# Kernel optimization log

Hardware: AMD Instinct MI355X
Metric: run time of the kernel (lower is better)

Reference implementation:

```python
import jax, jax.numpy as jnp
import numpy as np

SEQ_LEN = 4096
INPUT_SIZE = 1024
OUTPUT_SIZE = 1024


def _xavier(key, shape):
    n = shape[0]
    lim = 1.0 / (n ** 0.5)
    return jax.random.uniform(key, shape, minval=-lim, maxval=lim, dtype=jnp.float32)


def setup_inputs() -> dict:
    key = jax.random.key(0)
    kx, kk, kv, kq = jax.random.split(key, 4)
    X = jax.random.normal(kx, (SEQ_LEN, INPUT_SIZE), dtype=jnp.float32)
    Wk = _xavier(kk, (INPUT_SIZE, OUTPUT_SIZE))
    Wv = _xavier(kv, (INPUT_SIZE, OUTPUT_SIZE))
    Wq = _xavier(kq, (INPUT_SIZE, OUTPUT_SIZE))
    return {"X": X, "Wk": Wk, "Wv": Wv, "Wq": Wq}


def reference(X, Wk, Wv, Wq):
    # Faithful to original: scores = K @ Q^T (note K first, no 1/sqrt(d) scaling)
    K = X @ Wk  # (S, D)
    V = X @ Wv  # (S, D)
    Q = X @ Wq  # (S, D)
    scores = jnp.einsum('sd,td->st', K, Q)  # (S, S) == K @ Q^T
    attn = jax.nn.softmax(scores, axis=-1) @ V  # (S, D)
    return attn
```

## Files before the change

### kernel.cpp

```cpp
#include <hip/hip_runtime.h>
#include <hip/hip_fp16.h>
#include <cstdint>

#define SEQ 4096
#define DIM 1024

typedef _Float16 f16x8 __attribute__((ext_vector_type(8)));
typedef float f32x16 __attribute__((ext_vector_type(16)));
typedef __attribute__((address_space(1))) void as1_void;
typedef __attribute__((address_space(3))) void as3_void;

__device__ __forceinline__ ushort f2h(float f) {
  _Float16 h = (_Float16)f;
  return __builtin_bit_cast(ushort, h);
}

__global__ void convert_all_kernel(const float* __restrict__ X, const float* __restrict__ Wk,
                                   const float* __restrict__ Wv, const float* __restrict__ Wq,
                                   ushort* __restrict__ Xh, ushort* __restrict__ Wt) {
  const int z = blockIdx.z;
  const int tx = threadIdx.x, ty = threadIdx.y;
  if (z == 3) {
    const int bid = blockIdx.y * 32 + blockIdx.x;
    const int t = ty * 32 + tx;
#pragma unroll
    for (int k = 0; k < 4; k++) {
      int i = bid * 1024 + k * 256 + t;
      float4 v = reinterpret_cast<const float4*>(X)[i];
      ushort4 o = { f2h(v.x), f2h(v.y), f2h(v.z), f2h(v.w) };
      reinterpret_cast<ushort4*>(Xh)[i] = o;
    }
    return;
  }
  __shared__ float tile[32][33];
  const float* W = (z == 0) ? Wk : (z == 1) ? Wv : Wq;
  int n0 = blockIdx.x * 32, k0 = blockIdx.y * 32;
#pragma unroll
  for (int r = 0; r < 4; r++) {
    int k = ty + r * 8;
    tile[k][tx] = W[(size_t)(k0 + k) * DIM + n0 + tx];
  }
  __syncthreads();
  ushort* out = Wt + (size_t)z * DIM * DIM;
#pragma unroll
  for (int r = 0; r < 4; r++) {
    int n = ty + r * 8;
    out[(size_t)(n0 + n) * DIM + k0 + tx] = f2h(tile[tx][n]);
  }
}

template <bool F16_OUT>
__device__ __forceinline__ void gemm_tile(const ushort* __restrict__ A,
                                          const ushort* __restrict__ B,
                                          void* __restrict__ C,
                                          int N, int K, int m0, int n0,
                                          int kt0, int ktend) {
  constexpr int BK = 64;
  __shared__ __align__(16) ushort As[128 * BK];
  __shared__ __align__(16) ushort Bs[128 * BK];
  const int tid = threadIdx.x;
  const int wave = tid >> 6, lane = tid & 63;
  const int l31 = lane & 31, khalf = lane >> 5;
  const int wm = (wave & 1) * 64, wn = (wave >> 1) * 64;

  const int srow = tid >> 3;
  const int skey = ((srow & 7) ^ ((srow >> 3) & 3));
  const int sce = (((tid & 7) ^ skey) * 8);
  const int rk = (l31 & 7) ^ ((l31 >> 3) & 3);

  f32x16 acc[2][2];
#pragma unroll
  for (int i = 0; i < 2; i++)
#pragma unroll
    for (int j = 0; j < 2; j++)
#pragma unroll
      for (int r = 0; r < 16; r++) acc[i][j][r] = 0.f;

  for (int kt = kt0; kt < ktend; kt += BK) {
    __syncthreads();
#pragma unroll
    for (int q = 0; q < 4; q++) {
      const ushort* ga = A + (size_t)(m0 + srow + q * 32) * K + kt + sce;
      __builtin_amdgcn_global_load_lds((const as1_void*)ga,
                                       (as3_void*)&As[wave * 512 + q * 2048], 16, 0, 0);
    }
#pragma unroll
    for (int q = 0; q < 4; q++) {
      const ushort* gb = B + (size_t)(n0 + srow + q * 32) * K + kt + sce;
      __builtin_amdgcn_global_load_lds((const as1_void*)gb,
                                       (as3_void*)&Bs[wave * 512 + q * 2048], 16, 0, 0);
    }
    __syncthreads();
#pragma unroll
    for (int ks = 0; ks < 4; ks++) {
      f16x8 af[2], bfr[2];
      const int ck = (ks * 2 + khalf);
#pragma unroll
      for (int i = 0; i < 2; i++)
        af[i] = *reinterpret_cast<const f16x8*>(
            &As[(wm + i * 32 + l31) * BK + ((ck ^ rk) * 8)]);
#pragma unroll
      for (int j = 0; j < 2; j++)
        bfr[j] = *reinterpret_cast<const f16x8*>(
            &Bs[(wn + j * 32 + l31) * BK + ((ck ^ rk) * 8)]);
#pragma unroll
      for (int i = 0; i < 2; i++)
#pragma unroll
        for (int j = 0; j < 2; j++)
          acc[i][j] = __builtin_amdgcn_mfma_f32_32x32x16_f16(af[i], bfr[j], acc[i][j], 0, 0, 0);
    }
  }

#pragma unroll
  for (int i = 0; i < 2; i++)
#pragma unroll
    for (int j = 0; j < 2; j++)
#pragma unroll
      for (int r = 0; r < 16; r++) {
        int row = m0 + wm + i * 32 + (r & 3) + 8 * (r >> 2) + 4 * khalf;
        int col = n0 + wn + j * 32 + l31;
        if (F16_OUT)
          reinterpret_cast<ushort*>(C)[(size_t)row * N + col] = f2h(acc[i][j][r]);
        else
          reinterpret_cast<float*>(C)[(size_t)row * N + col] = acc[i][j][r];
      }
}

__device__ __forceinline__ void gemm_tile_w128(const ushort* __restrict__ A,
                                               const ushort* __restrict__ B,
                                               ushort* __restrict__ C,
                                               int N, int K, int m0, int n0,
                                               int kt0, int ktend) {
  constexpr int BK = 64;
  __shared__ __align__(16) ushort As[128 * BK];
  __shared__ __align__(16) ushort Bs[256 * BK];
  const int tid = threadIdx.x;
  const int wave = tid >> 6, lane = tid & 63;
  const int l31 = lane & 31, khalf = lane >> 5;
  const int wm = (wave & 1) * 64, wn = (wave >> 1) * 128;

  const int srow = tid >> 3;
  const int skey = ((srow & 7) ^ ((srow >> 3) & 3));
  const int sce = (((tid & 7) ^ skey) * 8);
  const int rk = (l31 & 7) ^ ((l31 >> 3) & 3);

  f32x16 acc[2][4];
#pragma unroll
  for (int i = 0; i < 2; i++)
#pragma unroll
    for (int j = 0; j < 4; j++)
#pragma unroll
      for (int r = 0; r < 16; r++) acc[i][j][r] = 0.f;

  for (int kt = kt0; kt < ktend; kt += BK) {
    __syncthreads();
#pragma unroll
    for (int q = 0; q < 4; q++) {
      const ushort* ga = A + (size_t)(m0 + srow + q * 32) * K + kt + sce;
      __builtin_amdgcn_global_load_lds((const as1_void*)ga,
                                       (as3_void*)&As[wave * 512 + q * 2048], 16, 0, 0);
    }
#pragma unroll
    for (int q = 0; q < 8; q++) {
      const ushort* gb = B + (size_t)(n0 + srow + q * 32) * K + kt + sce;
      __builtin_amdgcn_global_load_lds((const as1_void*)gb,
                                       (as3_void*)&Bs[wave * 512 + q * 2048], 16, 0, 0);
    }
    __syncthreads();
#pragma unroll
    for (int ks = 0; ks < 4; ks++) {
      f16x8 af[2], bfr[4];
      const int ck = (ks * 2 + khalf);
#pragma unroll
      for (int i = 0; i < 2; i++)
        af[i] = *reinterpret_cast<const f16x8*>(
            &As[(wm + i * 32 + l31) * BK + ((ck ^ rk) * 8)]);
#pragma unroll
      for (int j = 0; j < 4; j++)
        bfr[j] = *reinterpret_cast<const f16x8*>(
            &Bs[(wn + j * 32 + l31) * BK + ((ck ^ rk) * 8)]);
#pragma unroll
      for (int i = 0; i < 2; i++)
#pragma unroll
        for (int j = 0; j < 4; j++)
          acc[i][j] = __builtin_amdgcn_mfma_f32_32x32x16_f16(af[i], bfr[j], acc[i][j], 0, 0, 0);
    }
  }

#pragma unroll
  for (int i = 0; i < 2; i++)
#pragma unroll
    for (int j = 0; j < 4; j++)
#pragma unroll
      for (int r = 0; r < 16; r++) {
        int row = m0 + wm + i * 32 + (r & 3) + 8 * (r >> 2) + 4 * khalf;
        int col = n0 + wn + j * 32 + l31;
        C[(size_t)row * N + col] = f2h(acc[i][j][r]);
      }
}

__global__ __launch_bounds__(256) void proj_kernel(const ushort* __restrict__ Xh,
                                                   const ushort* __restrict__ Wt,
                                                   ushort* __restrict__ Kh,
                                                   ushort* __restrict__ Qh,
                                                   ushort* __restrict__ Vt) {
  const int z = blockIdx.z;
  const ushort* A;
  const ushort* B;
  ushort* C;
  int N, m0, n0;
  if (z < 2) {
    A = Xh;
    B = Wt + (size_t)(z == 0 ? 0 : 2) * DIM * DIM;
    C = (z == 0) ? Kh : Qh;
    N = DIM;
    m0 = (blockIdx.x >> 3) * 128;
    n0 = (blockIdx.x & 7) * 128;
  } else {
    A = Wt + (size_t)DIM * DIM;
    B = Xh;
    C = Vt;
    N = SEQ;
    m0 = (blockIdx.x >> 5) * 128;
    n0 = (blockIdx.x & 31) * 128;
  }
  gemm_tile<true>(A, B, C, N, DIM, m0, n0, 0, DIM);
}

__global__ __launch_bounds__(256, 2) void score_kernel(const ushort* __restrict__ Kh,
                                                       const ushort* __restrict__ Qh,
                                                       ushort* __restrict__ S) {
  const int f = blockIdx.x;
  const int xcd = f & 7;
  const int r = f >> 3;
  const int t = xcd * 64 + r;
  const int within = t & 63, st = t >> 6;
  const int sx = within & 7, sy = within >> 3;
  const int tx = (st & 1) * 8 + sx;
  const int ty = (st >> 1) * 8 + sy;
  gemm_tile_w128(Kh, Qh, S, SEQ, DIM, ty * 128, tx * 256, 0, DIM);
}

__global__ __launch_bounds__(256, 2) void out_splitk_kernel(const ushort* __restrict__ P,
                                                            const ushort* __restrict__ Vt,
                                                            ushort* __restrict__ Part) {
  const int f = blockIdx.x;
  const int z = f >> 7;
  const int q = f & 127;
  const int xcd = q & 7;
  const int r = q >> 3;
  const int t = xcd * 16 + r;
  const int tx = t & 3, ty = t >> 2;
  ushort* C = Part + (size_t)z * SEQ * DIM;
  gemm_tile_w128(P, Vt, C, DIM, SEQ, ty * 128, tx * 256,
                 z * (SEQ / 4), (z + 1) * (SEQ / 4));
}

__global__ void reduce4_kernel(const ushort* __restrict__ Part, float* __restrict__ out, int n8) {
  int i = blockIdx.x * blockDim.x + threadIdx.x;
  if (i >= n8) return;
  const f16x8* p0 = reinterpret_cast<const f16x8*>(Part);
  const f16x8* p1 = p0 + n8;
  const f16x8* p2 = p1 + n8;
  const f16x8* p3 = p2 + n8;
  f16x8 a = p0[i], b = p1[i], c = p2[i], d = p3[i];
  float4 lo, hi;
  lo.x = (float)a[0] + (float)b[0] + (float)c[0] + (float)d[0];
  lo.y = (float)a[1] + (float)b[1] + (float)c[1] + (float)d[1];
  lo.z = (float)a[2] + (float)b[2] + (float)c[2] + (float)d[2];
  lo.w = (float)a[3] + (float)b[3] + (float)c[3] + (float)d[3];
  hi.x = (float)a[4] + (float)b[4] + (float)c[4] + (float)d[4];
  hi.y = (float)a[5] + (float)b[5] + (float)c[5] + (float)d[5];
  hi.z = (float)a[6] + (float)b[6] + (float)c[6] + (float)d[6];
  hi.w = (float)a[7] + (float)b[7] + (float)c[7] + (float)d[7];
  reinterpret_cast<float4*>(out)[i * 2] = lo;
  reinterpret_cast<float4*>(out)[i * 2 + 1] = hi;
}

__global__ __launch_bounds__(256) void softmax_kernel(const ushort* __restrict__ S,
                                                      ushort* __restrict__ P) {
  const int wave = threadIdx.x >> 6, lane = threadIdx.x & 63;
  const int row = blockIdx.x * 4 + wave;
  const ushort* s = S + (size_t)row * SEQ;
  float v[64];
#pragma unroll
  for (int i = 0; i < 8; i++) {
    f16x8 h = reinterpret_cast<const f16x8*>(s)[i * 64 + lane];
#pragma unroll
    for (int j = 0; j < 8; j++) v[i * 8 + j] = (float)h[j];
  }
  float m = v[0];
#pragma unroll
  for (int j = 1; j < 64; j++) m = fmaxf(m, v[j]);
#pragma unroll
  for (int o = 32; o > 0; o >>= 1) m = fmaxf(m, __shfl_xor(m, o, 64));
  float sum = 0.f;
#pragma unroll
  for (int j = 0; j < 64; j++) {
    v[j] = __expf(v[j] - m);
    sum += v[j];
  }
#pragma unroll
  for (int o = 32; o > 0; o >>= 1) sum += __shfl_xor(sum, o, 64);
  float inv = 1.0f / sum;
  ushort* p = P + (size_t)row * SEQ;
#pragma unroll
  for (int i = 0; i < 8; i++) {
    f16x8 h;
#pragma unroll
    for (int j = 0; j < 8; j++) h[j] = (_Float16)(v[i * 8 + j] * inv);
    reinterpret_cast<f16x8*>(p)[i * 64 + lane] = h;
  }
}

extern "C" void kernel_launch(void* const* d_in, const int* in_sizes, int n_in,
                              void* d_out, int out_size, void* d_ws, size_t ws_size,
                              hipStream_t stream) {
  const float* X = (const float*)d_in[0];
  const float* Wk = (const float*)d_in[1];
  const float* Wv = (const float*)d_in[2];
  const float* Wq = (const float*)d_in[3];

  char* ws = (char*)d_ws;
  size_t off = 0;
  ushort* Xh = (ushort*)(ws + off); off += (size_t)SEQ * DIM * 2;
  ushort* Wt = (ushort*)(ws + off); off += (size_t)3 * DIM * DIM * 2;
  ushort* Kh = (ushort*)(ws + off); off += (size_t)SEQ * DIM * 2;
  ushort* Qh = (ushort*)(ws + off); off += (size_t)SEQ * DIM * 2;
  ushort* Vt = (ushort*)(ws + off); off += (size_t)SEQ * DIM * 2;
  ushort* S = (ushort*)(ws + off);  off += (size_t)SEQ * SEQ * 2;
  ushort* P = (ushort*)(ws + off);  off += (size_t)SEQ * SEQ * 2;

  ushort* Part = S;

  convert_all_kernel<<<dim3(32, 32, 4), dim3(32, 8), 0, stream>>>(X, Wk, Wv, Wq, Xh, Wt);
  proj_kernel<<<dim3(256, 1, 3), 256, 0, stream>>>(Xh, Wt, Kh, Qh, Vt);
  score_kernel<<<512, 256, 0, stream>>>(Kh, Qh, S);
  softmax_kernel<<<1024, 256, 0, stream>>>(S, P);
  out_splitk_kernel<<<512, 256, 0, stream>>>(P, Vt, Part);
  reduce4_kernel<<<SEQ * DIM / 8 / 256, 256, 0, stream>>>(Part, (float*)d_out, SEQ * DIM / 8);
}
```

Baseline: 210.2 us.

## Use 256x256 double-buffered GEMM tiles with 8 waves for all GEMMs

Replaces the two 128-row GEMM tile routines with a single 256x256 tile routine that runs 512 threads (8 waves, each computing 128x64) and double-buffers the A and B tiles in LDS. The loads for the next K slice are issued during the MFMA phase, with per-step barriers and setprio raised around the MFMAs. The projection, score and output GEMMs all switch to this tile and to new launch grids with XCD-aware block remapping. The aim is more data reuse per tile and load/compute overlap; the cost is 128KB of LDS per block, which limits occupancy, and fewer blocks (256) per launch, which can underfill the CUs.

```diff
diff --git a/kernel.cpp b/kernel.cpp
--- a/kernel.cpp
+++ b/kernel.cpp
@@ -49,148 +49,94 @@
   }
 }
 
-template <bool F16_OUT>
-__device__ __forceinline__ void gemm_tile(const ushort* __restrict__ A,
-                                          const ushort* __restrict__ B,
-                                          void* __restrict__ C,
-                                          int N, int K, int m0, int n0,
-                                          int kt0, int ktend) {
+__device__ __forceinline__ void gemm_tile256(const ushort* __restrict__ A,
+                                             const ushort* __restrict__ B,
+                                             ushort* __restrict__ C,
+                                             int N, int K, int m0, int n0,
+                                             int kt0, int ktend) {
   constexpr int BK = 64;
-  __shared__ __align__(16) ushort As[128 * BK];
-  __shared__ __align__(16) ushort Bs[128 * BK];
+  __shared__ __align__(16) ushort As[2][256 * BK];
+  __shared__ __align__(16) ushort Bs[2][256 * BK];
   const int tid = threadIdx.x;
   const int wave = tid >> 6, lane = tid & 63;
   const int l31 = lane & 31, khalf = lane >> 5;
-  const int wm = (wave & 1) * 64, wn = (wave >> 1) * 64;
+  const int wm = (wave & 1) * 128, wn = (wave >> 1) * 64;
 
   const int srow = tid >> 3;
   const int skey = ((srow & 7) ^ ((srow >> 3) & 3));
   const int sce = (((tid & 7) ^ skey) * 8);
   const int rk = (l31 & 7) ^ ((l31 >> 3) & 3);
 
-  f32x16 acc[2][2];
-#pragma unroll
-  for (int i = 0; i < 2; i++)
+  f32x16 acc[4][2];
+#pragma unroll
+  for (int i = 0; i < 4; i++)
 #pragma unroll
     for (int j = 0; j < 2; j++)
 #pragma unroll
       for (int r = 0; r < 16; r++) acc[i][j][r] = 0.f;
 
-  for (int kt = kt0; kt < ktend; kt += BK) {
-    __syncthreads();
-#pragma unroll
-    for (int q = 0; q < 4; q++) {
-      const ushort* ga = A + (size_t)(m0 + srow + q * 32) * K + kt + sce;
-      __builtin_amdgcn_global_load_lds((const as1_void*)ga,
-                                       (as3_void*)&As[wave * 512 + q * 2048], 16, 0, 0);
-    }
-#pragma unroll
-    for (int q = 0; q < 4; q++) {
-      const ushort* gb = B + (size_t)(n0 + srow + q * 32) * K + kt + sce;
-      __builtin_amdgcn_global_load_lds((const as1_void*)gb,
-                                       (as3_void*)&Bs[wave * 512 + q * 2048], 16, 0, 0);
+  const ushort* Abase = A + (size_t)(m0 + srow) * K + sce;
+  const ushort* Bbase = B + (size_t)(n0 + srow) * K + sce;
+  const int ldsbase = wave * 512;
+
+#pragma unroll
+  for (int q = 0; q < 4; q++)
+    __builtin_amdgcn_global_load_lds((const as1_void*)(Abase + (size_t)q * 64 * K + kt0),
+                                     (as3_void*)&As[0][ldsbase + q * 4096], 16, 0, 0);
+#pragma unroll
+  for (int q = 0; q < 4; q++)
+    __builtin_amdgcn_global_load_lds((const as1_void*)(Bbase + (size_t)q * 64 * K + kt0),
+                                     (as3_void*)&Bs[0][ldsbase + q * 4096], 16, 0, 0);
+  __syncthreads();
+
+  const int ntiles = (ktend - kt0) >> 6;
+  for (int tt = 0; tt < ntiles; ++tt) {
+    const int cur = tt & 1;
+    const int kt = kt0 + tt * BK;
+    const bool pf = (tt + 1 < ntiles);
+    const ushort* As_c = As[cur];
+    const ushort* Bs_c = Bs[cur];
+#pragma unroll
+    for (int ks = 0; ks < 4; ks++) {
+      f16x8 af[4], bf2[2];
+      const int co = (((ks * 2 + khalf) ^ rk) * 8);
+#pragma unroll
+      for (int i = 0; i < 4; i++)
+        af[i] = *reinterpret_cast<const f16x8*>(&As_c[(wm + i * 32 + l31) * BK + co]);
+#pragma unroll
+      for (int j = 0; j < 2; j++)
+        bf2[j] = *reinterpret_cast<const f16x8*>(&Bs_c[(wn + j * 32 + l31) * BK + co]);
+      if (pf && ks == 0) {
+#pragma unroll
+        for (int q = 0; q < 4; q++)
+          __builtin_amdgcn_global_load_lds(
+              (const as1_void*)(Abase + (size_t)q * 64 * K + kt + BK),
+              (as3_void*)&As[cur ^ 1][ldsbase + q * 4096], 16, 0, 0);
+      }
+      if (pf && ks == 1) {
+#pragma unroll
+        for (int q = 0; q < 4; q++)
+          __builtin_amdgcn_global_load_lds(
+              (const as1_void*)(Bbase + (size_t)q * 64 * K + kt + BK),
+              (as3_void*)&Bs[cur ^ 1][ldsbase + q * 4096], 16, 0, 0);
+      }
+      __builtin_amdgcn_s_barrier();
+      __builtin_amdgcn_s_setprio(1);
+#pragma unroll
+      for (int i = 0; i < 4; i++)
+#pragma unroll
+        for (int j = 0; j < 2; j++)
+          acc[i][j] = __builtin_amdgcn_mfma_f32_32x32x16_f16(af[i], bf2[j], acc[i][j], 0, 0, 0);
+      __builtin_amdgcn_s_setprio(0);
+      if (ks < 3) __builtin_amdgcn_s_barrier();
     }
     __syncthreads();
-#pragma unroll
-    for (int ks = 0; ks < 4; ks++) {
-      f16x8 af[2], bfr[2];
-      const int ck = (ks * 2 + khalf);
-#pragma unroll
-      for (int i = 0; i < 2; i++)
-        af[i] = *reinterpret_cast<const f16x8*>(
-            &As[(wm + i * 32 + l31) * BK + ((ck ^ rk) * 8)]);
-#pragma unroll
-      for (int j = 0; j < 2; j++)
-        bfr[j] = *reinterpret_cast<const f16x8*>(
-            &Bs[(wn + j * 32 + l31) * BK + ((ck ^ rk) * 8)]);
-#pragma unroll
-      for (int i = 0; i < 2; i++)
-#pragma unroll
-        for (int j = 0; j < 2; j++)
-          acc[i][j] = __builtin_amdgcn_mfma_f32_32x32x16_f16(af[i], bfr[j], acc[i][j], 0, 0, 0);
-    }
-  }
-
-#pragma unroll
-  for (int i = 0; i < 2; i++)
+  }
+
+#pragma unroll
+  for (int i = 0; i < 4; i++)
 #pragma unroll
     for (int j = 0; j < 2; j++)
-#pragma unroll
-      for (int r = 0; r < 16; r++) {
-        int row = m0 + wm + i * 32 + (r & 3) + 8 * (r >> 2) + 4 * khalf;
-        int col = n0 + wn + j * 32 + l31;
-        if (F16_OUT)
-          reinterpret_cast<ushort*>(C)[(size_t)row * N + col] = f2h(acc[i][j][r]);
-        else
-          reinterpret_cast<float*>(C)[(size_t)row * N + col] = acc[i][j][r];
-      }
-}
-
-__device__ __forceinline__ void gemm_tile_w128(const ushort* __restrict__ A,
-                                               const ushort* __restrict__ B,
-                                               ushort* __restrict__ C,
-                                               int N, int K, int m0, int n0,
-                                               int kt0, int ktend) {
-  constexpr int BK = 64;
-  __shared__ __align__(16) ushort As[128 * BK];
-  __shared__ __align__(16) ushort Bs[256 * BK];
-  const int tid = threadIdx.x;
-  const int wave = tid >> 6, lane = tid & 63;
-  const int l31 = lane & 31, khalf = lane >> 5;
-  const int wm = (wave & 1) * 64, wn = (wave >> 1) * 128;
-
-  const int srow = tid >> 3;
-  const int skey = ((srow & 7) ^ ((srow >> 3) & 3));
-  const int sce = (((tid & 7) ^ skey) * 8);
-  const int rk = (l31 & 7) ^ ((l31 >> 3) & 3);
-
-  f32x16 acc[2][4];
-#pragma unroll
-  for (int i = 0; i < 2; i++)
-#pragma unroll
-    for (int j = 0; j < 4; j++)
-#pragma unroll
-      for (int r = 0; r < 16; r++) acc[i][j][r] = 0.f;
-
-  for (int kt = kt0; kt < ktend; kt += BK) {
-    __syncthreads();
-#pragma unroll
-    for (int q = 0; q < 4; q++) {
-      const ushort* ga = A + (size_t)(m0 + srow + q * 32) * K + kt + sce;
-      __builtin_amdgcn_global_load_lds((const as1_void*)ga,
-                                       (as3_void*)&As[wave * 512 + q * 2048], 16, 0, 0);
-    }
-#pragma unroll
-    for (int q = 0; q < 8; q++) {
-      const ushort* gb = B + (size_t)(n0 + srow + q * 32) * K + kt + sce;
-      __builtin_amdgcn_global_load_lds((const as1_void*)gb,
-                                       (as3_void*)&Bs[wave * 512 + q * 2048], 16, 0, 0);
-    }
-    __syncthreads();
-#pragma unroll
-    for (int ks = 0; ks < 4; ks++) {
-      f16x8 af[2], bfr[4];
-      const int ck = (ks * 2 + khalf);
-#pragma unroll
-      for (int i = 0; i < 2; i++)
-        af[i] = *reinterpret_cast<const f16x8*>(
-            &As[(wm + i * 32 + l31) * BK + ((ck ^ rk) * 8)]);
-#pragma unroll
-      for (int j = 0; j < 4; j++)
-        bfr[j] = *reinterpret_cast<const f16x8*>(
-            &Bs[(wn + j * 32 + l31) * BK + ((ck ^ rk) * 8)]);
-#pragma unroll
-      for (int i = 0; i < 2; i++)
-#pragma unroll
-        for (int j = 0; j < 4; j++)
-          acc[i][j] = __builtin_amdgcn_mfma_f32_32x32x16_f16(af[i], bfr[j], acc[i][j], 0, 0, 0);
-    }
-  }
-
-#pragma unroll
-  for (int i = 0; i < 2; i++)
-#pragma unroll
-    for (int j = 0; j < 4; j++)
 #pragma unroll
       for (int r = 0; r < 16; r++) {
         int row = m0 + wm + i * 32 + (r & 3) + 8 * (r >> 2) + 4 * khalf;
@@ -199,61 +145,54 @@
       }
 }
 
-__global__ __launch_bounds__(256) void proj_kernel(const ushort* __restrict__ Xh,
-                                                   const ushort* __restrict__ Wt,
-                                                   ushort* __restrict__ Kh,
-                                                   ushort* __restrict__ Qh,
-                                                   ushort* __restrict__ Vt) {
-  const int z = blockIdx.z;
+__global__ __launch_bounds__(512, 2) void proj256_kernel(const ushort* __restrict__ Xh,
+                                                         const ushort* __restrict__ Wt,
+                                                         ushort* __restrict__ Kh,
+                                                         ushort* __restrict__ Qh,
+                                                         ushort* __restrict__ Vt) {
+  const int b = blockIdx.x;
   const ushort* A;
   const ushort* B;
-  ushort* C;
+  ushort* Cp;
   int N, m0, n0;
-  if (z < 2) {
+  if (b < 128) {
+    const int z = b >> 6, q = b & 63;
     A = Xh;
-    B = Wt + (size_t)(z == 0 ? 0 : 2) * DIM * DIM;
-    C = (z == 0) ? Kh : Qh;
+    B = Wt + (size_t)(z ? 2 : 0) * DIM * DIM;
+    Cp = z ? Qh : Kh;
     N = DIM;
-    m0 = (blockIdx.x >> 3) * 128;
-    n0 = (blockIdx.x & 7) * 128;
+    m0 = (q >> 2) * 256;
+    n0 = (q & 3) * 256;
   } else {
+    const int q = b - 128;
     A = Wt + (size_t)DIM * DIM;
     B = Xh;
-    C = Vt;
+    Cp = Vt;
     N = SEQ;
-    m0 = (blockIdx.x >> 5) * 128;
-    n0 = (blockIdx.x & 31) * 128;
-  }
-  gemm_tile<true>(A, B, C, N, DIM, m0, n0, 0, DIM);
-}
-
-__global__ __launch_bounds__(256, 2) void score_kernel(const ushort* __restrict__ Kh,
-                                                       const ushort* __restrict__ Qh,
-                                                       ushort* __restrict__ S) {
+    m0 = (q >> 4) * 256;
+    n0 = (q & 15) * 256;
+  }
+  gemm_tile256(A, B, Cp, N, DIM, m0, n0, 0, DIM);
+}
+
+__global__ __launch_bounds__(512, 2) void score256_kernel(const ushort* __restrict__ Kh,
+                                                          const ushort* __restrict__ Qh,
+                                                          ushort* __restrict__ S) {
   const int f = blockIdx.x;
-  const int xcd = f & 7;
-  const int r = f >> 3;
-  const int t = xcd * 64 + r;
-  const int within = t & 63, st = t >> 6;
-  const int sx = within & 7, sy = within >> 3;
-  const int tx = (st & 1) * 8 + sx;
-  const int ty = (st >> 1) * 8 + sy;
-  gemm_tile_w128(Kh, Qh, S, SEQ, DIM, ty * 128, tx * 256, 0, DIM);
-}
-
-__global__ __launch_bounds__(256, 2) void out_splitk_kernel(const ushort* __restrict__ P,
-                                                            const ushort* __restrict__ Vt,
-                                                            ushort* __restrict__ Part) {
+  const int t = (f & 7) * 32 + (f >> 3);
+  gemm_tile256(Kh, Qh, S, SEQ, DIM, (t >> 4) * 256, (t & 15) * 256, 0, DIM);
+}
+
+__global__ __launch_bounds__(512, 2) void out256_kernel(const ushort* __restrict__ P,
+                                                        const ushort* __restrict__ Vt,
+                                                        ushort* __restrict__ Part) {
   const int f = blockIdx.x;
-  const int z = f >> 7;
-  const int q = f & 127;
-  const int xcd = q & 7;
-  const int r = q >> 3;
-  const int t = xcd * 16 + r;
-  const int tx = t & 3, ty = t >> 2;
-  ushort* C = Part + (size_t)z * SEQ * DIM;
-  gemm_tile_w128(P, Vt, C, DIM, SEQ, ty * 128, tx * 256,
-                 z * (SEQ / 4), (z + 1) * (SEQ / 4));
+  const int z = f >> 6;
+  const int q = f & 63;
+  const int t = (q & 7) * 8 + (q >> 3);
+  ushort* Cp = Part + (size_t)z * SEQ * DIM;
+  gemm_tile256(P, Vt, Cp, DIM, SEQ, (t >> 2) * 256, (t & 3) * 256,
+               z * (SEQ / 4), (z + 1) * (SEQ / 4));
 }
 
 __global__ void reduce4_kernel(const ushort* __restrict__ Part, float* __restrict__ out, int n8) {
@@ -334,9 +273,9 @@
   ushort* Part = S;
 
   convert_all_kernel<<<dim3(32, 32, 4), dim3(32, 8), 0, stream>>>(X, Wk, Wv, Wq, Xh, Wt);
-  proj_kernel<<<dim3(256, 1, 3), 256, 0, stream>>>(Xh, Wt, Kh, Qh, Vt);
-  score_kernel<<<512, 256, 0, stream>>>(Kh, Qh, S);
+  proj256_kernel<<<256, 512, 0, stream>>>(Xh, Wt, Kh, Qh, Vt);
+  score256_kernel<<<256, 512, 0, stream>>>(Kh, Qh, S);
   softmax_kernel<<<1024, 256, 0, stream>>>(S, P);
-  out_splitk_kernel<<<512, 256, 0, stream>>>(P, Vt, Part);
+  out256_kernel<<<256, 512, 0, stream>>>(P, Vt, Part);
   reduce4_kernel<<<SEQ * DIM / 8 / 256, 256, 0, stream>>>(Part, (float*)d_out, SEQ * DIM / 8);
 }
```

Measured after the change: 208.1 us. No clear change (-1.0%).

## Double-buffer 256x256 score GEMM and drop split-K output with its reduce pass

Applied to the files above, without the earlier changes.

The score GEMM now uses 512-thread blocks computing 256x256 tiles with double-buffered LDS. The next K-tile is prefetched through global_load_lds while MFMAs run on the current one, with barriers and s_setprio around the MFMA groups. The P@V output GEMM drops the 4-way split-K, the fp16 partial buffers and the separate reduce kernel, and writes fp32 directly from 128x128 tiles over the full K. This cuts LDS-load stalls, a kernel launch and the partial-sum traffic. The cost is larger LDS use per block, lower occupancy, and a long serial K loop per output tile with only 256 blocks.

```diff
diff --git a/kernel.cpp b/kernel.cpp
--- a/kernel.cpp
+++ b/kernel.cpp
@@ -126,71 +126,93 @@
       }
 }
 
-__device__ __forceinline__ void gemm_tile_w128(const ushort* __restrict__ A,
-                                               const ushort* __restrict__ B,
-                                               ushort* __restrict__ C,
-                                               int N, int K, int m0, int n0,
-                                               int kt0, int ktend) {
+__device__ __forceinline__ void gemm_tile256(const ushort* __restrict__ A,
+                                             const ushort* __restrict__ B,
+                                             ushort* __restrict__ C,
+                                             int N, int K, int m0, int n0,
+                                             int kt0, int ktend) {
   constexpr int BK = 64;
-  __shared__ __align__(16) ushort As[128 * BK];
-  __shared__ __align__(16) ushort Bs[256 * BK];
+  __shared__ __align__(16) ushort As[2][256 * BK];
+  __shared__ __align__(16) ushort Bs[2][256 * BK];
   const int tid = threadIdx.x;
   const int wave = tid >> 6, lane = tid & 63;
   const int l31 = lane & 31, khalf = lane >> 5;
-  const int wm = (wave & 1) * 64, wn = (wave >> 1) * 128;
+  const int wm = (wave & 1) * 128, wn = (wave >> 1) * 64;
 
   const int srow = tid >> 3;
   const int skey = ((srow & 7) ^ ((srow >> 3) & 3));
   const int sce = (((tid & 7) ^ skey) * 8);
   const int rk = (l31 & 7) ^ ((l31 >> 3) & 3);
 
-  f32x16 acc[2][4];
-#pragma unroll
-  for (int i = 0; i < 2; i++)
-#pragma unroll
-    for (int j = 0; j < 4; j++)
+  f32x16 acc[4][2];
+#pragma unroll
+  for (int i = 0; i < 4; i++)
+#pragma unroll
+    for (int j = 0; j < 2; j++)
 #pragma unroll
       for (int r = 0; r < 16; r++) acc[i][j][r] = 0.f;
 
-  for (int kt = kt0; kt < ktend; kt += BK) {
+  const ushort* Abase = A + (size_t)(m0 + srow) * K + sce;
+  const ushort* Bbase = B + (size_t)(n0 + srow) * K + sce;
+  const int ldsbase = wave * 512;
+
+  const int ntiles = (ktend - kt0) >> 6;
+
+#pragma unroll
+  for (int q = 0; q < 4; q++)
+    __builtin_amdgcn_global_load_lds((const as1_void*)(Abase + (size_t)q * 64 * K + kt0),
+                                     (as3_void*)&As[0][ldsbase + q * 4096], 16, 0, 0);
+#pragma unroll
+  for (int q = 0; q < 4; q++)
+    __builtin_amdgcn_global_load_lds((const as1_void*)(Bbase + (size_t)q * 64 * K + kt0),
+                                     (as3_void*)&Bs[0][ldsbase + q * 4096], 16, 0, 0);
+  __syncthreads();
+
+  for (int tt = 0; tt < ntiles; ++tt) {
+    const int cur = tt & 1, nb = cur ^ 1;
+    const int nkt = kt0 + (tt + 1) * BK;
+    const bool pf = (tt + 1 < ntiles);
+    const ushort* As_c = As[cur];
+    const ushort* Bs_c = Bs[cur];
+#pragma unroll
+    for (int ks = 0; ks < 4; ks++) {
+      f16x8 af[4], bf2[2];
+      const int co = (((ks * 2 + khalf)) ^ rk) * 8;
+#pragma unroll
+      for (int i = 0; i < 4; i++)
+        af[i] = *reinterpret_cast<const f16x8*>(&As_c[(wm + i * 32 + l31) * BK + co]);
+#pragma unroll
+      for (int j = 0; j < 2; j++)
+        bf2[j] = *reinterpret_cast<const f16x8*>(&Bs_c[(wn + j * 32 + l31) * BK + co]);
+      if (pf && ks == 0) {
+#pragma unroll
+        for (int q = 0; q < 4; q++)
+          __builtin_amdgcn_global_load_lds((const as1_void*)(Abase + (size_t)q * 64 * K + nkt),
+                                           (as3_void*)&As[nb][ldsbase + q * 4096], 16, 0, 0);
+      }
+      if (pf && ks == 1) {
+#pragma unroll
+        for (int q = 0; q < 4; q++)
+          __builtin_amdgcn_global_load_lds((const as1_void*)(Bbase + (size_t)q * 64 * K + nkt),
+                                           (as3_void*)&Bs[nb][ldsbase + q * 4096], 16, 0, 0);
+      }
+      __builtin_amdgcn_s_barrier();
+      __builtin_amdgcn_s_setprio(1);
+#pragma unroll
+      for (int i = 0; i < 4; i++)
+#pragma unroll
+        for (int j = 0; j < 2; j++)
+          acc[i][j] = __builtin_amdgcn_mfma_f32_32x32x16_f16(af[i], bf2[j], acc[i][j], 0, 0, 0);
+      __builtin_amdgcn_s_setprio(0);
+      if (ks < 3) __builtin_amdgcn_s_barrier();
+    }
     __syncthreads();
-#pragma unroll
-    for (int q = 0; q < 4; q++) {
-      const ushort* ga = A + (size_t)(m0 + srow + q * 32) * K + kt + sce;
-      __builtin_amdgcn_global_load_lds((const as1_void*)ga,
-                                       (as3_void*)&As[wave * 512 + q * 2048], 16, 0, 0);
-    }
-#pragma unroll
-    for (int q = 0; q < 8; q++) {
-      const ushort* gb = B + (size_t)(n0 + srow + q * 32) * K + kt + sce;
-      __builtin_amdgcn_global_load_lds((const as1_void*)gb,
-                                       (as3_void*)&Bs[wave * 512 + q * 2048], 16, 0, 0);
-    }
-    __syncthreads();
-#pragma unroll
-    for (int ks = 0; ks < 4; ks++) {
-      f16x8 af[2], bfr[4];
-      const int ck = (ks * 2 + khalf);
-#pragma unroll
-      for (int i = 0; i < 2; i++)
-        af[i] = *reinterpret_cast<const f16x8*>(
-            &As[(wm + i * 32 + l31) * BK + ((ck ^ rk) * 8)]);
-#pragma unroll
-      for (int j = 0; j < 4; j++)
-        bfr[j] = *reinterpret_cast<const f16x8*>(
-            &Bs[(wn + j * 32 + l31) * BK + ((ck ^ rk) * 8)]);
-#pragma unroll
-      for (int i = 0; i < 2; i++)
-#pragma unroll
-        for (int j = 0; j < 4; j++)
-          acc[i][j] = __builtin_amdgcn_mfma_f32_32x32x16_f16(af[i], bfr[j], acc[i][j], 0, 0, 0);
-    }
-  }
-
-#pragma unroll
-  for (int i = 0; i < 2; i++)
-#pragma unroll
-    for (int j = 0; j < 4; j++)
+  }
+
+#pragma unroll
+  for (int i = 0; i < 4; i++)
+#pragma unroll
+    for (int j = 0; j < 2; j++)
 #pragma unroll
       for (int r = 0; r < 16; r++) {
         int row = m0 + wm + i * 32 + (r & 3) + 8 * (r >> 2) + 4 * khalf;
@@ -227,54 +249,12 @@
   gemm_tile<true>(A, B, C, N, DIM, m0, n0, 0, DIM);
 }
 
-__global__ __launch_bounds__(256, 2) void score_kernel(const ushort* __restrict__ Kh,
-                                                       const ushort* __restrict__ Qh,
-                                                       ushort* __restrict__ S) {
+__global__ __launch_bounds__(512, 2) void score256_kernel(const ushort* __restrict__ Kh,
+                                                          const ushort* __restrict__ Qh,
+                                                          ushort* __restrict__ S) {
   const int f = blockIdx.x;
-  const int xcd = f & 7;
-  const int r = f >> 3;
-  const int t = xcd * 64 + r;
-  const int within = t & 63, st = t >> 6;
-  const int sx = within & 7, sy = within >> 3;
-  const int tx = (st & 1) * 8 + sx;
-  const int ty = (st >> 1) * 8 + sy;
-  gemm_tile_w128(Kh, Qh, S, SEQ, DIM, ty * 128, tx * 256, 0, DIM);
-}
-
-__global__ __launch_bounds__(256, 2) void out_splitk_kernel(const ushort* __restrict__ P,
-                                                            const ushort* __restrict__ Vt,
-                                                            ushort* __restrict__ Part) {
-  const int f = blockIdx.x;
-  const int z = f >> 7;
-  const int q = f & 127;
-  const int xcd = q & 7;
-  const int r = q >> 3;
-  const int t = xcd * 16 + r;
-  const int tx = t & 3, ty = t >> 2;
-  ushort* C = Part + (size_t)z * SEQ * DIM;
-  gemm_tile_w128(P, Vt, C, DIM, SEQ, ty * 128, tx * 256,
-                 z * (SEQ / 4), (z + 1) * (SEQ / 4));
-}
-
-__global__ void reduce4_kernel(const ushort* __restrict__ Part, float* __restrict__ out, int n8) {
-  int i = blockIdx.x * blockDim.x + threadIdx.x;
-  if (i >= n8) return;
-  const f16x8* p0 = reinterpret_cast<const f16x8*>(Part);
-  const f16x8* p1 = p0 + n8;
-  const f16x8* p2 = p1 + n8;
-  const f16x8* p3 = p2 + n8;
-  f16x8 a = p0[i], b = p1[i], c = p2[i], d = p3[i];
-  float4 lo, hi;
-  lo.x = (float)a[0] + (float)b[0] + (float)c[0] + (float)d[0];
-  lo.y = (float)a[1] + (float)b[1] + (float)c[1] + (float)d[1];
-  lo.z = (float)a[2] + (float)b[2] + (float)c[2] + (float)d[2];
-  lo.w = (float)a[3] + (float)b[3] + (float)c[3] + (float)d[3];
-  hi.x = (float)a[4] + (float)b[4] + (float)c[4] + (float)d[4];
-  hi.y = (float)a[5] + (float)b[5] + (float)c[5] + (float)d[5];
-  hi.z = (float)a[6] + (float)b[6] + (float)c[6] + (float)d[6];
-  hi.w = (float)a[7] + (float)b[7] + (float)c[7] + (float)d[7];
-  reinterpret_cast<float4*>(out)[i * 2] = lo;
-  reinterpret_cast<float4*>(out)[i * 2 + 1] = hi;
+  const int t = (f & 7) * 32 + (f >> 3);
+  gemm_tile256(Kh, Qh, S, SEQ, DIM, (t >> 4) * 256, (t & 15) * 256, 0, DIM);
 }
 
 __global__ __launch_bounds__(256) void softmax_kernel(const ushort* __restrict__ S,
@@ -311,6 +291,15 @@
     for (int j = 0; j < 8; j++) h[j] = (_Float16)(v[i * 8 + j] * inv);
     reinterpret_cast<f16x8*>(p)[i * 64 + lane] = h;
   }
+}
+
+__global__ __launch_bounds__(256, 2) void out128_kernel(const ushort* __restrict__ P,
+                                                        const ushort* __restrict__ Vt,
+                                                        float* __restrict__ O) {
+  const int f = blockIdx.x;
+  const int t = (f & 7) * 32 + (f >> 3);
+  const int mt = t >> 3, nt = t & 7;
+  gemm_tile<false>(P, Vt, O, DIM, SEQ, mt * 128, nt * 128, 0, SEQ);
 }
 
 extern "C" void kernel_launch(void* const* d_in, const int* in_sizes, int n_in,
@@ -331,12 +320,9 @@
   ushort* S = (ushort*)(ws + off);  off += (size_t)SEQ * SEQ * 2;
   ushort* P = (ushort*)(ws + off);  off += (size_t)SEQ * SEQ * 2;
 
-  ushort* Part = S;
-
   convert_all_kernel<<<dim3(32, 32, 4), dim3(32, 8), 0, stream>>>(X, Wk, Wv, Wq, Xh, Wt);
   proj_kernel<<<dim3(256, 1, 3), 256, 0, stream>>>(Xh, Wt, Kh, Qh, Vt);
-  score_kernel<<<512, 256, 0, stream>>>(Kh, Qh, S);
+  score256_kernel<<<256, 512, 0, stream>>>(Kh, Qh, S);
   softmax_kernel<<<1024, 256, 0, stream>>>(S, P);
-  out_splitk_kernel<<<512, 256, 0, stream>>>(P, Vt, Part);
-  reduce4_kernel<<<SEQ * DIM / 8 / 256, 256, 0, stream>>>(Part, (float*)d_out, SEQ * DIM / 8);
-}
+  out128_kernel<<<256, 256, 0, stream>>>(P, Vt, (float*)d_out);
+}
```

Result: slower. 221.1 us (+5.2%).
